# Kernel optimization log

Hardware: AMD Instinct MI355X
Metric: run time of the kernel (lower is better)

Reference implementation:

```python
import jax, jax.numpy as jnp
import numpy as np

NV, NSEG, SEGSZ, GRID = 778, 16, 49, 32
SCALE_FACTOR = 0.1


def grid_sample_3d(vol, pts):
    """Trilinear grid_sample, align_corners=True, zeros padding.
    vol: [D,H,W]; pts: [N,3] with (x,y,z) in [-1,1] (x indexes W, z indexes D).
    """
    D, H, W = vol.shape
    fx = (pts[:, 0] + 1.0) * 0.5 * (W - 1)
    fy = (pts[:, 1] + 1.0) * 0.5 * (H - 1)
    fz = (pts[:, 2] + 1.0) * 0.5 * (D - 1)
    x0f, y0f, z0f = jnp.floor(fx), jnp.floor(fy), jnp.floor(fz)
    wx, wy, wz = fx - x0f, fy - y0f, fz - z0f
    x0 = x0f.astype(jnp.int32)
    y0 = y0f.astype(jnp.int32)
    z0 = z0f.astype(jnp.int32)
    out = jnp.zeros(pts.shape[0], vol.dtype)
    for dz in (0, 1):
        zz = z0 + dz
        ww_z = wz if dz else (1.0 - wz)
        for dy in (0, 1):
            yy = y0 + dy
            ww_zy = ww_z * (wy if dy else (1.0 - wy))
            for dx in (0, 1):
                xx = x0 + dx
                w = ww_zy * (wx if dx else (1.0 - wx))
                valid = (xx >= 0) & (xx < W) & (yy >= 0) & (yy < H) & (zz >= 0) & (zz < D)
                v = vol[jnp.clip(zz, 0, D - 1), jnp.clip(yy, 0, H - 1), jnp.clip(xx, 0, W - 1)]
                out = out + jnp.where(valid, v, 0.0) * w
    return out


def _boxes(segv):
    # segv: [B,16,S,3] -> center [B,16,3], scale [B,16]  (no_grad in original)
    mn = segv.min(axis=2)
    mx = segv.max(axis=2)
    center = 0.5 * (mn + mx)                       # mean of (min, max)
    scale = (1.0 + SCALE_FACTOR) * 0.5 * (mx - mn).max(axis=-1)
    return jax.lax.stop_gradient(center), jax.lax.stop_gradient(scale)


def _cross_sample(seg_src, center, scale, phi, seg):
    # seg_src [B,I,S,3]; center [B,J,3]; scale [B,J]; phi [J,B,G,G,G]
    B = seg_src.shape[0]
    coords = (seg_src[:, :, None, :, :] - center[:, None, :, None, :]) / scale[:, None, :, None, None]
    pts = coords.transpose(2, 0, 1, 3, 4).reshape(NSEG, B, NSEG * SEGSZ, 3)  # [J,B,M,3]
    vals = jax.vmap(jax.vmap(grid_sample_3d))(phi, pts)                      # [J,B,M]
    vals = vals.reshape(NSEG, B, NSEG, SEGSZ).transpose(1, 2, 0, 3)          # [B,I,J,S]
    phisum = vals.sum(axis=2)                                                # [B,I,S]
    orisum = (vals * scale[:, None, :, None]).sum(axis=2)                    # [B,I,S]
    flat = seg.reshape(-1)
    out = jnp.zeros((B, NV), jnp.float32).at[:, flat].add(phisum.reshape(B, -1))
    ori = jnp.zeros((B, NV), jnp.float32).at[:, flat].add(orisum.reshape(B, -1))
    return out, ori


def setup_inputs() -> dict:
    key = jax.random.key(0)
    k1, k2, k3, k4 = jax.random.split(key, 4)
    bs = 128
    vertices = jax.random.normal(k1, (bs, 2, NV, 3), dtype=jnp.float32)
    seg = jax.random.randint(k2, (NSEG, SEGSZ), 0, NV).astype(jnp.int32)
    phi_right = jax.random.uniform(k3, (NSEG, bs, GRID, GRID, GRID), dtype=jnp.float32)
    phi_left = jax.random.uniform(k4, (NSEG, bs, GRID, GRID, GRID), dtype=jnp.float32)
    return {"vertices": vertices, "phi_right": phi_right, "phi_left": phi_left, "seg": seg}


def reference(vertices, phi_right, phi_left, seg):
    left_vert = vertices[:, 1]   # [B,778,3]
    right_vert = vertices[:, 0]
    segL = left_vert[:, seg]     # [B,16,S,3]
    segR = right_vert[:, seg]
    cL, sL = _boxes(segL)
    cR, sR = _boxes(segR)
    out_left, _ = _cross_sample(segL, cR, sR, phi_right, seg)
    out_right, _ = _cross_sample(segR, cL, sL, phi_left, seg)
    num_hand = 2
    loss = (out_left / num_hand ** 2 + out_right / num_hand ** 2).sum(axis=1)  # [B]
    return loss
```

## Files before the change

kernel.cpp:

```cpp
#include <hip/hip_runtime.h>

#define NVV   778
#define NSEG  16
#define SEGSZ 49
#define GRIDN 32
#define BATCH 128
#define NPTS  (NSEG * SEGSZ)
#define VOLSZ (GRIDN * GRIDN * GRIDN)
#define NBLK  256
#define VPB   16

#define HF (16 * 1024)

typedef float f4v __attribute__((ext_vector_type(4)));

#define NTLD(p) __builtin_nontemporal_load((const f4v*)(p))

#define STAGE(DST, SRC) { \
    const float* s_ = (SRC) + (wv << 11) + (lane << 2); \
    float*       d_ = (DST) + (wv << 11) + (lane << 2); \
    f4v c0 = NTLD(s_ + 0 * 256); \
    f4v c1 = NTLD(s_ + 1 * 256); \
    f4v c2 = NTLD(s_ + 2 * 256); \
    f4v c3 = NTLD(s_ + 3 * 256); \
    f4v c4 = NTLD(s_ + 4 * 256); \
    f4v c5 = NTLD(s_ + 5 * 256); \
    f4v c6 = NTLD(s_ + 6 * 256); \
    f4v c7 = NTLD(s_ + 7 * 256); \
    *(f4v*)(d_ + 0 * 256) = c0; \
    *(f4v*)(d_ + 1 * 256) = c1; \
    *(f4v*)(d_ + 2 * 256) = c2; \
    *(f4v*)(d_ + 3 * 256) = c3; \
    *(f4v*)(d_ + 4 * 256) = c4; \
    *(f4v*)(d_ + 5 * 256) = c5; \
    *(f4v*)(d_ + 6 * 256) = c6; \
    *(f4v*)(d_ + 7 * 256) = c7; }

__device__ __forceinline__ float tapxy(const float* slab, int x0, int y0,
                                       float wx, float wy)
{
    float s = 0.f;
    #pragma unroll
    for (int dy = 0; dy < 2; ++dy) {
        int yy = y0 + dy;
        if (yy < 0 || yy >= GRIDN) continue;
        float wyv = dy ? wy : 1.f - wy;
        const float* row = slab + yy * GRIDN;
        #pragma unroll
        for (int dx = 0; dx < 2; ++dx) {
            int xx = x0 + dx;
            if (xx < 0 || xx >= GRIDN) continue;
            s += wyv * (dx ? wx : 1.f - wx) * row[xx];
        }
    }
    return s;
}

__global__ __launch_bounds__(1024, 4) void sample_kernel(
    const float* __restrict__ vertices, const int* __restrict__ seg,
    const float* __restrict__ phiR, const float* __restrict__ phiL,
    float* __restrict__ loss)
{
    __shared__ __align__(16) float B0[HF];
    __shared__ __align__(16) float B1[HF];
    __shared__ float4 sbox[VPB];
    __shared__ float wsum[8];

    const int tid  = threadIdx.x;
    const int bx   = blockIdx.x;
    const int k    = bx & (NSEG - 1);
    const int wv   = tid >> 6;
    const int lane = tid & 63;
    const bool producer = (wv < 8);
    const int ct   = tid - 512;

    auto phiPtr = [&](int it) {
        int vid  = bx + NBLK * it;
        int b    = (vid >> 4) & (BATCH - 1);
        int pass = vid >> 11;
        return (pass == 0 ? phiR : phiL) + ((size_t)k * BATCH + b) * VOLSZ;
    };
    auto vertBase = [&](int it) {
        int vid  = bx + NBLK * it;
        int b    = (vid >> 4) & (BATCH - 1);
        int srcS = (vid >> 11) == 0 ? 1 : 0;
        return vertices + ((size_t)b * 2 + srcS) * NVV * 3;
    };

    int pvi1 = 0, pvi2 = 0;
    bool has2 = false;
    if (!producer) {
        pvi1 = seg[ct];
        has2 = (ct + 512) < NPTS;
        pvi2 = has2 ? seg[ct + 512] : 0;
    }

    {
        int vidw    = bx + NBLK * wv;
        int bbw     = (vidw >> 4) & (BATCH - 1);
        int boxSide = ((vidw >> 11) == 0) ? 0 : 1;
        bool bact   = lane < SEGSZ;
        int bvi     = bact ? seg[k * SEGSZ + lane] : 0;
        const float* bvp = vertices + (((size_t)bbw * 2 + boxSide) * NVV + bvi) * 3;
        float x = bvp[0], y = bvp[1], z = bvp[2];
        float mnx = bact ? x : 1e30f, mxx = bact ? x : -1e30f;
        float mny = bact ? y : 1e30f, mxy = bact ? y : -1e30f;
        float mnz = bact ? z : 1e30f, mxz = bact ? z : -1e30f;
        #pragma unroll
        for (int m = 32; m; m >>= 1) {
            mnx = fminf(mnx, __shfl_xor(mnx, m));
            mxx = fmaxf(mxx, __shfl_xor(mxx, m));
            mny = fminf(mny, __shfl_xor(mny, m));
            mxy = fmaxf(mxy, __shfl_xor(mxy, m));
            mnz = fminf(mnz, __shfl_xor(mnz, m));
            mxz = fmaxf(mxz, __shfl_xor(mxz, m));
        }
        if (lane == 0) {
            float ext = fmaxf(fmaxf(mxx - mnx, mxy - mny), mxz - mnz);
            sbox[wv] = make_float4(0.5f * (mnx + mxx), 0.5f * (mny + mxy),
                                   0.5f * (mnz + mxz), 1.0f / (0.55f * ext));
        }
    }

    float p1x = 0.f, p1y = 0.f, p1z = 0.f;
    float p2x = 0.f, p2y = 0.f, p2z = 0.f;
    if (!producer) {
        const float* vb = vertBase(0);
        p1x = vb[pvi1 * 3 + 0]; p1y = vb[pvi1 * 3 + 1]; p1z = vb[pvi1 * 3 + 2];
        if (has2) {
            p2x = vb[pvi2 * 3 + 0]; p2y = vb[pvi2 * 3 + 1]; p2z = vb[pvi2 * 3 + 2];
        }
    }

    if (producer) { STAGE(B0, phiPtr(0)) }

    __syncthreads();

    float n1x = 0.f, n1y = 0.f, n1z = 0.f;
    float n2x = 0.f, n2y = 0.f, n2z = 0.f;

    for (int v = 0; v < VPB; ++v) {
        const bool more = (v + 1 < VPB);

        float f1x = 0.f, f1y = 0.f, f1z = -2.f;
        float f2x = 0.f, f2y = 0.f, f2z = -2.f;
        if (!producer) {
            float4 b4 = sbox[v];
            f1x = ((p1x - b4.x) * b4.w + 1.f) * 15.5f;
            f1y = ((p1y - b4.y) * b4.w + 1.f) * 15.5f;
            f1z = ((p1z - b4.z) * b4.w + 1.f) * 15.5f;
            if (has2) {
                f2x = ((p2x - b4.x) * b4.w + 1.f) * 15.5f;
                f2y = ((p2y - b4.y) * b4.w + 1.f) * 15.5f;
                f2z = ((p2z - b4.z) * b4.w + 1.f) * 15.5f;
            }
        }
        bool a1 = (f1x > -1.f && f1x < 32.f && f1y > -1.f && f1y < 32.f &&
                   f1z > -1.f && f1z < 32.f);
        bool a2 = (f2x > -1.f && f2x < 32.f && f2y > -1.f && f2y < 32.f &&
                   f2z > -1.f && f2z < 32.f);
        float x1f = floorf(f1x), y1f = floorf(f1y), z1f = floorf(f1z);
        float x2f = floorf(f2x), y2f = floorf(f2y), z2f = floorf(f2z);
        float w1x = f1x - x1f, w1y = f1y - y1f, w1z = f1z - z1f;
        float w2x = f2x - x2f, w2y = f2y - y2f, w2z = f2z - z2f;
        int x1 = (int)x1f, y1 = (int)y1f, z1 = (int)z1f;
        int x2 = (int)x2f, y2 = (int)y2f, z2 = (int)z2f;
        float acc1 = 0.f, acc2 = 0.f;

        if (producer) {
            STAGE(B1, phiPtr(v) + HF)
        } else {
            if (v > 0 && ct == 0) {
                float tot = 0.f;
                #pragma unroll
                for (int i = 0; i < 8; ++i) tot += wsum[i];
                int vidp = bx + NBLK * (v - 1);
                atomicAdd(loss + ((vidp >> 4) & (BATCH - 1)), tot * 0.25f);
            }
            if (a1 && z1 <= 15) {
                if (z1 >= 0)
                    acc1 += (1.f - w1z) * tapxy(B0 + z1 * 1024, x1, y1, w1x, w1y);
                if (z1 <= 14)
                    acc1 += w1z * tapxy(B0 + (z1 + 1) * 1024, x1, y1, w1x, w1y);
            }
            if (a2 && z2 <= 15) {
                if (z2 >= 0)
                    acc2 += (1.f - w2z) * tapxy(B0 + z2 * 1024, x2, y2, w2x, w2y);
                if (z2 <= 14)
                    acc2 += w2z * tapxy(B0 + (z2 + 1) * 1024, x2, y2, w2x, w2y);
            }
            if (more) {
                const float* vb = vertBase(v + 1);
                n1x = vb[pvi1 * 3 + 0]; n1y = vb[pvi1 * 3 + 1]; n1z = vb[pvi1 * 3 + 2];
                if (has2) {
                    n2x = vb[pvi2 * 3 + 0]; n2y = vb[pvi2 * 3 + 1]; n2z = vb[pvi2 * 3 + 2];
                }
            }
        }
        __syncthreads();

        if (producer) {
            if (more) { STAGE(B0, phiPtr(v + 1)) }
        } else {
            if (a1 && z1 >= 15) {
                if (z1 >= 16)
                    acc1 += (1.f - w1z) * tapxy(B1 + (z1 - 16) * 1024, x1, y1, w1x, w1y);
                if (z1 <= 30)
                    acc1 += w1z * tapxy(B1 + (z1 - 15) * 1024, x1, y1, w1x, w1y);
            }
            if (a2 && z2 >= 15) {
                if (z2 >= 16)
                    acc2 += (1.f - w2z) * tapxy(B1 + (z2 - 16) * 1024, x2, y2, w2x, w2y);
                if (z2 <= 30)
                    acc2 += w2z * tapxy(B1 + (z2 - 15) * 1024, x2, y2, w2x, w2y);
            }
            float acc = acc1 + acc2;
            #pragma unroll
            for (int off = 32; off; off >>= 1)
                acc += __shfl_down(acc, off);
            if (lane == 0) wsum[wv - 8] = acc;
        }
        __syncthreads();
        p1x = n1x; p1y = n1y; p1z = n1z;
        p2x = n2x; p2y = n2y; p2z = n2z;
    }

    if (!producer && ct == 0) {
        float tot = 0.f;
        #pragma unroll
        for (int i = 0; i < 8; ++i) tot += wsum[i];
        int vidp = bx + NBLK * (VPB - 1);
        atomicAdd(loss + ((vidp >> 4) & (BATCH - 1)), tot * 0.25f);
    }
}

extern "C" void kernel_launch(void* const* d_in, const int* in_sizes, int n_in,
                              void* d_out, int out_size, void* d_ws, size_t ws_size,
                              hipStream_t stream) {
    const float* vertices = (const float*)d_in[0];
    const float* phiR     = (const float*)d_in[1];
    const float* phiL     = (const float*)d_in[2];
    const int*   seg      = (const int*)d_in[3];
    float* loss = (float*)d_out;

    hipMemsetAsync(d_out, 0, (size_t)out_size * sizeof(float), stream);

    sample_kernel<<<NBLK, 1024, 0, stream>>>(vertices, seg, phiR, phiL, loss);
}
```

Before: 102.3 us.

## Split volume staging into four quarter-slabs with 512-thread blocks and more blocks

```diff
diff --git a/kernel.cpp b/kernel.cpp
--- a/kernel.cpp
+++ b/kernel.cpp
@@ -5,15 +5,13 @@
 #define SEGSZ 49
 #define GRIDN 32
 #define BATCH 128
-#define NPTS  (NSEG * SEGSZ)
+#define NPTS  784
 #define VOLSZ (GRIDN * GRIDN * GRIDN)
-#define NBLK  256
-#define VPB   16
-
-#define HF (16 * 1024)
+#define NBLK  512
+#define VPB   8
+#define PFLT  8192
 
 typedef float f4v __attribute__((ext_vector_type(4)));
-
 #define NTLD(p) __builtin_nontemporal_load((const f4v*)(p))
 
 #define STAGE(DST, SRC) { \
@@ -56,23 +54,44 @@
     return s;
 }
 
-__global__ __launch_bounds__(1024, 4) void sample_kernel(
+#define TAP1(Q, BASE, J) \
+    if (a##J) { \
+        if (z##J >= 0 && (z##J >> 3) == (Q)) \
+            acc##J += (1.f - w##J##z) * tapxy((BASE) + (z##J - 8 * (Q)) * 1024, x##J, y##J, w##J##x, w##J##y); \
+        if ((z##J + 1) <= 31 && ((z##J + 1) >> 3) == (Q)) \
+            acc##J += w##J##z * tapxy((BASE) + (z##J + 1 - 8 * (Q)) * 1024, x##J, y##J, w##J##x, w##J##y); \
+    }
+#define TAPALL(Q, BASE) \
+    TAP1(Q, BASE, 1) TAP1(Q, BASE, 2) TAP1(Q, BASE, 3) \
+    if (has4) { TAP1(Q, BASE, 4) }
+
+#define SETUP(J, PX, PY, PZ) { \
+    float fx = ((PX) - b4.x) * b4.w * 15.5f + 15.5f; \
+    float fy = ((PY) - b4.y) * b4.w * 15.5f + 15.5f; \
+    float fz = ((PZ) - b4.z) * b4.w * 15.5f + 15.5f; \
+    a##J = (fx > -1.f && fx < 32.f && fy > -1.f && fy < 32.f && \
+            fz > -1.f && fz < 32.f); \
+    float xf = floorf(fx), yf = floorf(fy), zf = floorf(fz); \
+    w##J##x = fx - xf; w##J##y = fy - yf; w##J##z = fz - zf; \
+    x##J = (int)xf; y##J = (int)yf; z##J = (int)zf; acc##J = 0.f; }
+
+__global__ __launch_bounds__(512, 4) void sample_kernel(
     const float* __restrict__ vertices, const int* __restrict__ seg,
     const float* __restrict__ phiR, const float* __restrict__ phiL,
     float* __restrict__ loss)
 {
-    __shared__ __align__(16) float B0[HF];
-    __shared__ __align__(16) float B1[HF];
+    __shared__ __align__(16) float P0[PFLT];
+    __shared__ __align__(16) float P1[PFLT];
     __shared__ float4 sbox[VPB];
-    __shared__ float wsum[8];
+    __shared__ float wsum[4];
 
     const int tid  = threadIdx.x;
     const int bx   = blockIdx.x;
     const int k    = bx & (NSEG - 1);
     const int wv   = tid >> 6;
     const int lane = tid & 63;
-    const bool producer = (wv < 8);
-    const int ct   = tid - 512;
+    const bool producer = (wv < 4);
+    const int ct   = tid - 256;
 
     auto phiPtr = [&](int it) {
         int vid  = bx + NBLK * it;
@@ -86,13 +105,16 @@
         int srcS = (vid >> 11) == 0 ? 1 : 0;
         return vertices + ((size_t)b * 2 + srcS) * NVV * 3;
     };
-
-    int pvi1 = 0, pvi2 = 0;
-    bool has2 = false;
+    auto bOf = [&](int it) { return ((bx + NBLK * it) >> 4) & (BATCH - 1); };
+
+    int pvi1 = 0, pvi2 = 0, pvi3 = 0, pvi4 = 0;
+    bool has4 = false;
     if (!producer) {
         pvi1 = seg[ct];
-        has2 = (ct + 512) < NPTS;
-        pvi2 = has2 ? seg[ct + 512] : 0;
+        pvi2 = seg[ct + 256];
+        pvi3 = seg[ct + 512];
+        has4 = (ct + 768) < NPTS;
+        pvi4 = has4 ? seg[ct + 768] : 0;
     }
 
     {
@@ -122,115 +144,89 @@
         }
     }
 
-    float p1x = 0.f, p1y = 0.f, p1z = 0.f;
-    float p2x = 0.f, p2y = 0.f, p2z = 0.f;
-    if (!producer) {
+    float p1x = 0.f, p1y = 0.f, p1z = 0.f, p2x = 0.f, p2y = 0.f, p2z = 0.f;
+    float p3x = 0.f, p3y = 0.f, p3z = 0.f, p4x = 0.f, p4y = 0.f, p4z = 0.f;
+    if (producer) {
+        STAGE(P0, phiPtr(0))
+    } else {
         const float* vb = vertBase(0);
-        p1x = vb[pvi1 * 3 + 0]; p1y = vb[pvi1 * 3 + 1]; p1z = vb[pvi1 * 3 + 2];
-        if (has2) {
-            p2x = vb[pvi2 * 3 + 0]; p2y = vb[pvi2 * 3 + 1]; p2z = vb[pvi2 * 3 + 2];
-        }
-    }
-
-    if (producer) { STAGE(B0, phiPtr(0)) }
-
+        p1x = vb[pvi1 * 3]; p1y = vb[pvi1 * 3 + 1]; p1z = vb[pvi1 * 3 + 2];
+        p2x = vb[pvi2 * 3]; p2y = vb[pvi2 * 3 + 1]; p2z = vb[pvi2 * 3 + 2];
+        p3x = vb[pvi3 * 3]; p3y = vb[pvi3 * 3 + 1]; p3z = vb[pvi3 * 3 + 2];
+        if (has4) {
+            p4x = vb[pvi4 * 3]; p4y = vb[pvi4 * 3 + 1]; p4z = vb[pvi4 * 3 + 2];
+        }
+    }
     __syncthreads();
 
-    float n1x = 0.f, n1y = 0.f, n1z = 0.f;
-    float n2x = 0.f, n2y = 0.f, n2z = 0.f;
+    float n1x = 0.f, n1y = 0.f, n1z = 0.f, n2x = 0.f, n2y = 0.f, n2z = 0.f;
+    float n3x = 0.f, n3y = 0.f, n3z = 0.f, n4x = 0.f, n4y = 0.f, n4z = 0.f;
 
     for (int v = 0; v < VPB; ++v) {
         const bool more = (v + 1 < VPB);
-
-        float f1x = 0.f, f1y = 0.f, f1z = -2.f;
-        float f2x = 0.f, f2y = 0.f, f2z = -2.f;
-        if (!producer) {
+        bool a1 = false, a2 = false, a3 = false, a4 = false;
+        int x1, y1, z1, x2, y2, z2, x3, y3, z3, x4, y4, z4;
+        float w1x, w1y, w1z, w2x, w2y, w2z, w3x, w3y, w3z, w4x, w4y, w4z;
+        float acc1 = 0.f, acc2 = 0.f, acc3 = 0.f, acc4 = 0.f;
+
+        if (producer) {
+            STAGE(P1, phiPtr(v) + PFLT)
+        } else {
+            if (v > 0 && ct == 0) {
+                float tot = wsum[0] + wsum[1] + wsum[2] + wsum[3];
+                atomicAdd(loss + bOf(v - 1), tot * 0.25f);
+            }
             float4 b4 = sbox[v];
-            f1x = ((p1x - b4.x) * b4.w + 1.f) * 15.5f;
-            f1y = ((p1y - b4.y) * b4.w + 1.f) * 15.5f;
-            f1z = ((p1z - b4.z) * b4.w + 1.f) * 15.5f;
-            if (has2) {
-                f2x = ((p2x - b4.x) * b4.w + 1.f) * 15.5f;
-                f2y = ((p2y - b4.y) * b4.w + 1.f) * 15.5f;
-                f2z = ((p2z - b4.z) * b4.w + 1.f) * 15.5f;
-            }
-        }
-        bool a1 = (f1x > -1.f && f1x < 32.f && f1y > -1.f && f1y < 32.f &&
-                   f1z > -1.f && f1z < 32.f);
-        bool a2 = (f2x > -1.f && f2x < 32.f && f2y > -1.f && f2y < 32.f &&
-                   f2z > -1.f && f2z < 32.f);
-        float x1f = floorf(f1x), y1f = floorf(f1y), z1f = floorf(f1z);
-        float x2f = floorf(f2x), y2f = floorf(f2y), z2f = floorf(f2z);
-        float w1x = f1x - x1f, w1y = f1y - y1f, w1z = f1z - z1f;
-        float w2x = f2x - x2f, w2y = f2y - y2f, w2z = f2z - z2f;
-        int x1 = (int)x1f, y1 = (int)y1f, z1 = (int)z1f;
-        int x2 = (int)x2f, y2 = (int)y2f, z2 = (int)z2f;
-        float acc1 = 0.f, acc2 = 0.f;
-
-        if (producer) {
-            STAGE(B1, phiPtr(v) + HF)
-        } else {
-            if (v > 0 && ct == 0) {
-                float tot = 0.f;
-                #pragma unroll
-                for (int i = 0; i < 8; ++i) tot += wsum[i];
-                int vidp = bx + NBLK * (v - 1);
-                atomicAdd(loss + ((vidp >> 4) & (BATCH - 1)), tot * 0.25f);
-            }
-            if (a1 && z1 <= 15) {
-                if (z1 >= 0)
-                    acc1 += (1.f - w1z) * tapxy(B0 + z1 * 1024, x1, y1, w1x, w1y);
-                if (z1 <= 14)
-                    acc1 += w1z * tapxy(B0 + (z1 + 1) * 1024, x1, y1, w1x, w1y);
-            }
-            if (a2 && z2 <= 15) {
-                if (z2 >= 0)
-                    acc2 += (1.f - w2z) * tapxy(B0 + z2 * 1024, x2, y2, w2x, w2y);
-                if (z2 <= 14)
-                    acc2 += w2z * tapxy(B0 + (z2 + 1) * 1024, x2, y2, w2x, w2y);
-            }
+            SETUP(1, p1x, p1y, p1z)
+            SETUP(2, p2x, p2y, p2z)
+            SETUP(3, p3x, p3y, p3z)
+            if (has4) { SETUP(4, p4x, p4y, p4z) }
+            TAPALL(0, P0)
+        }
+        __syncthreads();
+
+        if (producer) {
+            STAGE(P0, phiPtr(v) + 2 * PFLT)
+        } else {
+            TAPALL(1, P1)
+        }
+        __syncthreads();
+
+        if (producer) {
+            STAGE(P1, phiPtr(v) + 3 * PFLT)
+        } else {
+            TAPALL(2, P0)
             if (more) {
                 const float* vb = vertBase(v + 1);
-                n1x = vb[pvi1 * 3 + 0]; n1y = vb[pvi1 * 3 + 1]; n1z = vb[pvi1 * 3 + 2];
-                if (has2) {
-                    n2x = vb[pvi2 * 3 + 0]; n2y = vb[pvi2 * 3 + 1]; n2z = vb[pvi2 * 3 + 2];
+                n1x = vb[pvi1 * 3]; n1y = vb[pvi1 * 3 + 1]; n1z = vb[pvi1 * 3 + 2];
+                n2x = vb[pvi2 * 3]; n2y = vb[pvi2 * 3 + 1]; n2z = vb[pvi2 * 3 + 2];
+                n3x = vb[pvi3 * 3]; n3y = vb[pvi3 * 3 + 1]; n3z = vb[pvi3 * 3 + 2];
+                if (has4) {
+                    n4x = vb[pvi4 * 3]; n4y = vb[pvi4 * 3 + 1]; n4z = vb[pvi4 * 3 + 2];
                 }
             }
         }
         __syncthreads();
 
         if (producer) {
-            if (more) { STAGE(B0, phiPtr(v + 1)) }
-        } else {
-            if (a1 && z1 >= 15) {
-                if (z1 >= 16)
-                    acc1 += (1.f - w1z) * tapxy(B1 + (z1 - 16) * 1024, x1, y1, w1x, w1y);
-                if (z1 <= 30)
-                    acc1 += w1z * tapxy(B1 + (z1 - 15) * 1024, x1, y1, w1x, w1y);
-            }
-            if (a2 && z2 >= 15) {
-                if (z2 >= 16)
-                    acc2 += (1.f - w2z) * tapxy(B1 + (z2 - 16) * 1024, x2, y2, w2x, w2y);
-                if (z2 <= 30)
-                    acc2 += w2z * tapxy(B1 + (z2 - 15) * 1024, x2, y2, w2x, w2y);
-            }
-            float acc = acc1 + acc2;
+            if (more) { STAGE(P0, phiPtr(v + 1)) }
+        } else {
+            TAPALL(3, P1)
+            float acc = acc1 + acc2 + acc3 + acc4;
             #pragma unroll
             for (int off = 32; off; off >>= 1)
                 acc += __shfl_down(acc, off);
-            if (lane == 0) wsum[wv - 8] = acc;
-        }
-        __syncthreads();
-        p1x = n1x; p1y = n1y; p1z = n1z;
-        p2x = n2x; p2y = n2y; p2z = n2z;
+            if (lane == 0) wsum[wv - 4] = acc;
+        }
+        __syncthreads();
+
+        p1x = n1x; p1y = n1y; p1z = n1z; p2x = n2x; p2y = n2y; p2z = n2z;
+        p3x = n3x; p3y = n3y; p3z = n3z; p4x = n4x; p4y = n4y; p4z = n4z;
     }
 
     if (!producer && ct == 0) {
-        float tot = 0.f;
-        #pragma unroll
-        for (int i = 0; i < 8; ++i) tot += wsum[i];
-        int vidp = bx + NBLK * (VPB - 1);
-        atomicAdd(loss + ((vidp >> 4) & (BATCH - 1)), tot * 0.25f);
+        float tot = wsum[0] + wsum[1] + wsum[2] + wsum[3];
+        atomicAdd(loss + bOf(VPB - 1), tot * 0.25f);
     }
 }
 
@@ -245,5 +241,5 @@
 
     hipMemsetAsync(d_out, 0, (size_t)out_size * sizeof(float), stream);
 
-    sample_kernel<<<NBLK, 1024, 0, stream>>>(vertices, seg, phiR, phiL, loss);
+    sample_kernel<<<NBLK, 512, 0, stream>>>(vertices, seg, phiR, phiL, loss);
 }
```

Result: no change. 101.4 us (median of 2 runs) (-0.9%).
